# Optimization experiments

Hardware: AMD Instinct MI355X
Metric: run time of the kernel (lower is better)

The kernel has to match this reference:

```python
import jax, jax.numpy as jnp
import numpy as np

N_HEADS = 16
ROPE_THETA = 10000.0


def _rotate_half(x):
    d = x.shape[-1] // 2
    return jnp.concatenate([-x[..., d:], x[..., :d]], axis=-1)


def setup_inputs() -> dict:
    key = jax.random.key(0)
    k1, k2, k3, k4 = jax.random.split(key, 4)
    B, S, D = 2, 2048, 2048
    std = 0.02
    return {
        "x": jax.random.normal(k1, (B, S, D), dtype=jnp.float32),
        "wq": std * jax.random.normal(k2, (D, D), dtype=jnp.float32),
        "wkv": std * jax.random.normal(k3, (D, 2 * D), dtype=jnp.float32),
        "wo": std * jax.random.normal(k4, (D, D), dtype=jnp.float32),
    }


def reference(x, wq, wkv, wo):
    # prefill case: kv_cache=None, past_length=0
    B, S, D = x.shape
    H = N_HEADS
    dh = D // H

    Q = x @ wq.T                                   # [B,S,D]
    K, V = jnp.split(x @ wkv, 2, axis=-1)          # [B,S,D] each

    q = Q.reshape(B, S, H, dh).transpose(0, 2, 1, 3)  # [B,H,S,dh]
    k = K.reshape(B, S, H, dh).transpose(0, 2, 1, 3)
    v = V.reshape(B, S, H, dh).transpose(0, 2, 1, 3)

    # RoPE tables (cos/sin of outer(pos, inv_freq), duplicated across halves)
    inv_freq = 1.0 / (ROPE_THETA ** (jnp.arange(0, dh, 2, dtype=jnp.float32) / dh))
    emb = jnp.arange(S, dtype=jnp.float32)[:, None] * inv_freq[None, :]  # [S, dh/2]
    cos = jnp.tile(jnp.cos(emb), (1, 2))[None, None]  # [1,1,S,dh]
    sin = jnp.tile(jnp.sin(emb), (1, 2))[None, None]

    q = q * cos + _rotate_half(q) * sin
    k = k * cos + _rotate_half(k) * sin

    scale = 1.0 / jnp.sqrt(jnp.asarray(dh, dtype=x.dtype))
    scores = jnp.einsum('bhqd,bhkd->bhqk', q, k) * scale  # [B,H,S,S]
    causal = jnp.tril(jnp.ones((S, S), dtype=bool))
    scores = jnp.where(causal[None, None], scores, -jnp.inf)
    attn = jax.nn.softmax(scores, axis=-1)

    out = jnp.einsum('bhqk,bhkd->bhqd', attn, v)          # [B,H,S,dh]
    out = out.transpose(0, 2, 1, 3).reshape(B, S, D)
    return out @ wo.T
```

## Files before the change

kernel.cpp:

```cpp
#include <hip/hip_runtime.h>
#include <stdint.h>

typedef unsigned short u16;
typedef __attribute__((ext_vector_type(8))) short short8;
typedef __attribute__((ext_vector_type(4))) float floatx4;

#define MFMA16(a, b, c) __builtin_amdgcn_mfma_f32_16x16x32_bf16(a, b, c, 0, 0, 0)

static __device__ __forceinline__ void gl_lds16(const void* g, void* l) {
  __builtin_amdgcn_global_load_lds(
      (const __attribute__((address_space(1))) uint32_t*)g,
      (__attribute__((address_space(3))) uint32_t*)l, 16, 0, 0);
}

static __device__ __forceinline__ float b2f(u16 u) {
  union { float f; unsigned u; } v;
  v.u = ((unsigned)u) << 16;
  return v.f;
}
static __device__ __forceinline__ u16 f2b(float f) {
  union { float f; unsigned u; } v;
  v.f = f;
  unsigned r = v.u + 0x7fffu + ((v.u >> 16) & 1u);
  return (u16)(r >> 16);
}

template <int CTRL>
static __device__ __forceinline__ float dppf(float x) {
  return __builtin_bit_cast(
      float, __builtin_amdgcn_update_dpp(0, __builtin_bit_cast(int, x), CTRL,
                                         0xF, 0xF, true));
}
static __device__ __forceinline__ float sum16(float x) {
  x += dppf<0x128>(x);
  x += dppf<0x124>(x);
  x += dppf<0x122>(x);
  x += dppf<0x121>(x);
  return x;
}
static __device__ __forceinline__ float max16(float x) {
  x = fmaxf(x, dppf<0x128>(x));
  x = fmaxf(x, dppf<0x124>(x));
  x = fmaxf(x, dppf<0x122>(x));
  x = fmaxf(x, dppf<0x121>(x));
  return x;
}

__global__ __launch_bounds__(256) void detect_f32(const u16* __restrict__ x,
                                                  int* __restrict__ flag) {
  __shared__ int cnt[256];
  int c = 0;
  for (int i = threadIdx.x; i < 65536; i += 256) {
    int e = (x[i] >> 7) & 0xFF;
    if (e >= 140) ++c;
  }
  cnt[threadIdx.x] = c;
  __syncthreads();
  for (int s = 128; s > 0; s >>= 1) {
    if (threadIdx.x < (unsigned)s) cnt[threadIdx.x] += cnt[threadIdx.x + s];
    __syncthreads();
  }
  if (threadIdx.x == 0) *flag = (cnt[0] > 1000) ? 1 : 0;
}

__global__ __launch_bounds__(256) void convert_in8(const void* __restrict__ src,
                                                   u16* __restrict__ dst, int n8,
                                                   const int* __restrict__ flag) {
  int i = blockIdx.x * 256 + threadIdx.x;
  if (i >= n8) return;
  short8 r;
  if (*flag) {
    const float4* s = (const float4*)src;
    float4 a = s[2 * i], b = s[2 * i + 1];
    r[0] = (short)f2b(a.x); r[1] = (short)f2b(a.y);
    r[2] = (short)f2b(a.z); r[3] = (short)f2b(a.w);
    r[4] = (short)f2b(b.x); r[5] = (short)f2b(b.y);
    r[6] = (short)f2b(b.z); r[7] = (short)f2b(b.w);
  } else {
    r = ((const short8*)src)[i];
  }
  ((short8*)dst)[i] = r;
}

__global__ __launch_bounds__(256) void transpose_conv(const void* __restrict__ in,
                                                      u16* __restrict__ out,
                                                      int R, int Ccols,
                                                      const int* __restrict__ flag) {
  __shared__ u16 tile[32][33];
  int f = *flag;
  int c0 = blockIdx.x * 32, r0 = blockIdx.y * 32;
  int lx = threadIdx.x & 31, ly = threadIdx.x >> 5;
#pragma unroll
  for (int i = 0; i < 32; i += 8) {
    size_t idx = (size_t)(r0 + ly + i) * Ccols + c0 + lx;
    tile[ly + i][lx] = f ? f2b(((const float*)in)[idx]) : ((const u16*)in)[idx];
  }
  __syncthreads();
#pragma unroll
  for (int i = 0; i < 32; i += 8)
    out[(size_t)(c0 + ly + i) * R + r0 + lx] = tile[lx][ly + i];
}

__global__ __launch_bounds__(256) void transpose_v(const u16* __restrict__ KV,
                                                   u16* __restrict__ Vt) {
  __shared__ u16 tile[32][33];
  int b = blockIdx.z;
  int d0 = blockIdx.x * 32, s0 = blockIdx.y * 32;
  int lx = threadIdx.x & 31, ly = threadIdx.x >> 5;
  const u16* src = KV + ((size_t)(b * 2048 + s0)) * 4096 + 2048 + d0;
#pragma unroll
  for (int i = 0; i < 32; i += 8)
    tile[ly + i][lx] = src[(size_t)(ly + i) * 4096 + lx];
  __syncthreads();
  u16* dst = Vt + ((size_t)(b * 2048 + d0)) * 2048 + s0;
#pragma unroll
  for (int i = 0; i < 32; i += 8)
    dst[(size_t)(ly + i) * 2048 + lx] = tile[lx][ly + i];
}

__global__ __launch_bounds__(256) void gemm_nt(const u16* __restrict__ A,
                                               const u16* __restrict__ Bm,
                                               void* __restrict__ Cv,
                                               int M, int N, int K,
                                               const int* __restrict__ flag,
                                               int flag_mode) {
  __shared__ u16 Ash[128 * 64];
  __shared__ u16 Bsh[128 * 64];
  int tid = threadIdx.x, w = tid >> 6, lane = tid & 63;
  int quad = lane >> 4, l15 = lane & 15;
  int m0 = blockIdx.y * 128, n0 = blockIdx.x * 128;
  int wm = (w & 1) * 64, wn = (w >> 1) * 64;
  int f32out = flag_mode ? *flag : 0;

  floatx4 acc[4][4];
#pragma unroll
  for (int i = 0; i < 4; ++i)
#pragma unroll
    for (int j = 0; j < 4; ++j) acc[i][j] = floatx4{0.f, 0.f, 0.f, 0.f};

  int srow = lane >> 3;
  int gch = (lane & 7) ^ srow;
  const u16* Ag = A + (size_t)(m0 + w * 32 + srow) * K + gch * 8;
  const u16* Bg = Bm + (size_t)(n0 + w * 32 + srow) * K + gch * 8;

  for (int k0 = 0; k0 < K; k0 += 64) {
    __syncthreads();
#pragma unroll
    for (int t = 0; t < 4; ++t) {
      gl_lds16(Ag + (size_t)t * 8 * K + k0, (void*)(Ash + (w * 32 + t * 8) * 64));
      gl_lds16(Bg + (size_t)t * 8 * K + k0, (void*)(Bsh + (w * 32 + t * 8) * 64));
    }
    __syncthreads();
#pragma unroll
    for (int kk = 0; kk < 2; ++kk) {
      int c = kk * 4 + quad;
      short8 af[4], bf[4];
#pragma unroll
      for (int i = 0; i < 4; ++i) {
        int m = wm + 16 * i + l15;
        af[i] = *(const short8*)(Ash + m * 64 + ((c ^ (m & 7)) << 3));
        int n = wn + 16 * i + l15;
        bf[i] = *(const short8*)(Bsh + n * 64 + ((c ^ (n & 7)) << 3));
      }
#pragma unroll
      for (int i = 0; i < 4; ++i)
#pragma unroll
        for (int j = 0; j < 4; ++j) acc[i][j] = MFMA16(af[i], bf[j], acc[i][j]);
    }
  }

#pragma unroll
  for (int i = 0; i < 4; ++i)
#pragma unroll
    for (int r = 0; r < 4; ++r) {
      int row = m0 + wm + 16 * i + quad * 4 + r;
      if (f32out) {
        float* cp = (float*)Cv + (size_t)row * N + n0 + wn + l15;
#pragma unroll
        for (int j = 0; j < 4; ++j) cp[16 * j] = acc[i][j][r];
      } else {
        u16* cp = (u16*)Cv + (size_t)row * N + n0 + wn + l15;
#pragma unroll
        for (int j = 0; j < 4; ++j) cp[16 * j] = f2b(acc[i][j][r]);
      }
    }
}

__global__ __launch_bounds__(256) void rope_kernel(u16* __restrict__ Q,
                                                   u16* __restrict__ KV) {
  const float scale = 0.08838834764831845f;
  int idx = blockIdx.x * 256 + threadIdx.x;
  int tok = idx >> 10;
  int rem = idx & 1023;
  int h = rem >> 6, i = rem & 63;
  int pos = tok & 2047;
  float f = __powf(10000.0f, -(float)(2 * i) * (1.0f / 128.0f));
  float ang = (float)pos * f;
  float s, c;
  sincosf(ang, &s, &c);

  size_t qb = (size_t)tok * 2048 + h * 128 + i;
  float q1 = b2f(Q[qb]), q2 = b2f(Q[qb + 64]);
  Q[qb] = f2b((q1 * c - q2 * s) * scale);
  Q[qb + 64] = f2b((q2 * c + q1 * s) * scale);

  size_t kb = (size_t)tok * 4096 + h * 128 + i;
  float k1 = b2f(KV[kb]), k2 = b2f(KV[kb + 64]);
  KV[kb] = f2b(k1 * c - k2 * s);
  KV[kb + 64] = f2b(k2 * c + k1 * s);
}

__global__ __launch_bounds__(512, 1) void flash_attn(const u16* __restrict__ Q,
                                                     const u16* __restrict__ KV,
                                                     const u16* __restrict__ Vt,
                                                     u16* __restrict__ O) {
  const int S = 2048, D = 2048, KVld = 4096;
  int bh = blockIdx.x;
  int pair = blockIdx.y;
  int b = bh >> 4, h = bh & 15;
  int tid = threadIdx.x, w = tid >> 6, lane = tid & 63;
  int quad = lane >> 4, l15 = lane & 15;

  const u16* Qb = Q + (size_t)(b * S) * D + h * 128;
  const u16* Kb = KV + (size_t)(b * S) * KVld + h * 128;
  const u16* Vtb = Vt + ((size_t)(b * 2048 + h * 128)) * S;

  __shared__ u16 Ksh[64 * 128];
  __shared__ u16 Vsh[128 * 64];
  __shared__ u16 Psh[8][16 * 64];

  for (int pi = 0; pi < 2; ++pi) {
    int qt = pi ? (15 - pair) : pair;
    int q0 = qt * 128;
    int qw = q0 + w * 16;

    short8 qf[4];
    {
      const u16* qp = Qb + (size_t)(qw + l15) * D + quad * 8;
#pragma unroll
      for (int kk = 0; kk < 4; ++kk) qf[kk] = *(const short8*)(qp + kk * 32);
    }

    floatx4 o[8];
#pragma unroll
    for (int t = 0; t < 8; ++t) o[t] = floatx4{0.f, 0.f, 0.f, 0.f};
    float mrow[4], lrow[4];
#pragma unroll
    for (int r = 0; r < 4; ++r) { mrow[r] = -1e30f; lrow[r] = 0.f; }

    int nk = 2 * qt + 2;
    for (int kt = 0; kt < nk; ++kt) {
      int kb = kt * 64;
      __syncthreads();

#pragma unroll
      for (int tt = 0; tt < 2; ++tt) {
        int r0 = w * 8 + tt * 4;
        int row = r0 + quad;
        int g = (l15 & 8) | ((l15 & 7) ^ (row & 7));
        gl_lds16(Kb + (size_t)(kb + row) * KVld + g * 8, (void*)(Ksh + r0 * 128));
      }
#pragma unroll
      for (int tt = 0; tt < 2; ++tt) {
        int d0 = w * 16 + tt * 8;
        int d = d0 + (lane >> 3);
        int g = (lane & 7) ^ (d & 7);
        gl_lds16(Vtb + (size_t)d * S + kb + g * 8, (void*)(Vsh + d0 * 64));
      }
      __syncthreads();

      if (kb <= qw + 15) {
        floatx4 sc[4];
#pragma unroll
        for (int nf = 0; nf < 4; ++nf) sc[nf] = floatx4{0.f, 0.f, 0.f, 0.f};
#pragma unroll
        for (int kk = 0; kk < 4; ++kk) {
          int c = kk * 4 + quad;
          short8 kf[4];
#pragma unroll
          for (int nf = 0; nf < 4; ++nf) {
            int n = nf * 16 + l15;
            int pc = (c & 8) | ((c & 7) ^ (n & 7));
            kf[nf] = *(const short8*)(Ksh + n * 128 + pc * 8);
          }
#pragma unroll
          for (int nf = 0; nf < 4; ++nf) sc[nf] = MFMA16(qf[kk], kf[nf], sc[nf]);
        }

        bool masked = (kb + 63 > qw);
        floatx4 alv;
#pragma unroll
        for (int r = 0; r < 4; ++r) {
          int qg = qw + quad * 4 + r;
          float v0 = sc[0][r], v1 = sc[1][r];
          float v2 = sc[2][r], v3 = sc[3][r];
          if (masked) {
            v0 = (kb + l15 <= qg) ? v0 : -1e30f;
            v1 = (kb + 16 + l15 <= qg) ? v1 : -1e30f;
            v2 = (kb + 32 + l15 <= qg) ? v2 : -1e30f;
            v3 = (kb + 48 + l15 <= qg) ? v3 : -1e30f;
          }
          float mx = max16(fmaxf(fmaxf(v0, v1), fmaxf(v2, v3)));
          float mn = fmaxf(mrow[r], mx);
          float al = __expf(mrow[r] - mn);
          mrow[r] = mn;
          float p0 = __expf(v0 - mn), p1 = __expf(v1 - mn);
          float p2 = __expf(v2 - mn), p3 = __expf(v3 - mn);
          float rs = sum16((p0 + p1) + (p2 + p3));
          lrow[r] = lrow[r] * al + rs;
          alv[r] = al;
          int m_ = quad * 4 + r, sw = m_ & 7;
          int cb = l15 >> 3, e = l15 & 7;
          u16* pr = Psh[w] + m_ * 64;
          pr[(((0 + cb) ^ sw) << 3) + e] = f2b(p0);
          pr[(((2 + cb) ^ sw) << 3) + e] = f2b(p1);
          pr[(((4 + cb) ^ sw) << 3) + e] = f2b(p2);
          pr[(((6 + cb) ^ sw) << 3) + e] = f2b(p3);
        }
#pragma unroll
        for (int t = 0; t < 8; ++t) o[t] *= alv;
        __asm__ volatile("s_waitcnt lgkmcnt(0)" ::: "memory");

#pragma unroll
        for (int ks = 0; ks < 2; ++ks) {
          int c = ks * 4 + quad;
          short8 pf = *(const short8*)(Psh[w] + l15 * 64 + ((c ^ (l15 & 7)) << 3));
#pragma unroll
          for (int t = 0; t < 8; ++t) {
            int d = t * 16 + l15;
            short8 vf = *(const short8*)(Vsh + d * 64 + ((c ^ (d & 7)) << 3));
            o[t] = MFMA16(pf, vf, o[t]);
          }
        }
      }
    }

#pragma unroll
    for (int r = 0; r < 4; ++r) {
      float inv = 1.0f / lrow[r];
      int qg = qw + quad * 4 + r;
      u16* op = O + (size_t)(b * S + qg) * D + h * 128;
#pragma unroll
      for (int t = 0; t < 8; ++t) op[t * 16 + l15] = f2b(o[t][r] * inv);
    }
  }
}

extern "C" void kernel_launch(void* const* d_in, const int* in_sizes, int n_in,
                              void* d_out, int out_size, void* d_ws, size_t ws_size,
                              hipStream_t stream) {
  const void* x = d_in[0];
  const void* wq = d_in[1];
  const void* wkv = d_in[2];
  const void* wo = d_in[3];

  int* flag = (int*)d_ws;
  u16* xb = (u16*)d_ws + 64;
  u16* Wbuf = xb + (size_t)8388608;
  u16* Qb = Wbuf + (size_t)8388608;
  u16* KVb = Qb + (size_t)8388608;
  u16* AO = xb;

  detect_f32<<<1, 256, 0, stream>>>((const u16*)x, flag);
  convert_in8<<<4096, 256, 0, stream>>>(x, xb, 1048576, flag);
  convert_in8<<<2048, 256, 0, stream>>>(wq, Wbuf, 524288, flag);
  gemm_nt<<<dim3(16, 32), 256, 0, stream>>>(xb, Wbuf, Qb, 4096, 2048, 2048, flag, 0);
  transpose_conv<<<dim3(128, 64), 256, 0, stream>>>(wkv, Wbuf, 2048, 4096, flag);
  gemm_nt<<<dim3(32, 32), 256, 0, stream>>>(xb, Wbuf, KVb, 4096, 4096, 2048, flag, 0);
  transpose_v<<<dim3(64, 64, 2), 256, 0, stream>>>(KVb, Wbuf);
  rope_kernel<<<16384, 256, 0, stream>>>(Qb, KVb);
  flash_attn<<<dim3(32, 8), 512, 0, stream>>>(Qb, KVb, Wbuf, AO);
  convert_in8<<<2048, 256, 0, stream>>>(wo, Wbuf, 524288, flag);
  gemm_nt<<<dim3(16, 32), 256, 0, stream>>>(AO, Wbuf, d_out, 4096, 2048, 2048, flag, 1);
}
```

Measured before the change: 488.9 us.

## Replace GEMM with 256x256 double-buffered, 8-wave pipelined MFMA kernel

Replaces the 128x128 single-buffered GEMM with a 256x256-tile, 512-thread kernel. It double-buffers LDS, issues global-to-LDS loads in quarter stages interleaved with MFMA phases, and uses explicit waitcnt, barriers and setprio. The goal is to hide global load latency and raise arithmetic intensity per tile for the three projection GEMMs. In exchange, LDS use per block is much larger, the grid has fewer blocks (128 or 256 blocks on a large CU count), and the hand-written waitcnt and barrier scheduling is fragile.

```diff
diff --git a/kernel.cpp b/kernel.cpp
--- a/kernel.cpp
+++ b/kernel.cpp
@@ -118,59 +118,156 @@
     dst[(size_t)(ly + i) * 2048 + lx] = tile[lx][ly + i];
 }
 
-__global__ __launch_bounds__(256) void gemm_nt(const u16* __restrict__ A,
-                                               const u16* __restrict__ Bm,
-                                               void* __restrict__ Cv,
-                                               int M, int N, int K,
-                                               const int* __restrict__ flag,
-                                               int flag_mode) {
-  __shared__ u16 Ash[128 * 64];
-  __shared__ u16 Bsh[128 * 64];
+__global__ __launch_bounds__(512, 2) void gemm8(const u16* __restrict__ A,
+                                                const u16* __restrict__ Bm,
+                                                void* __restrict__ Cv,
+                                                int M, int N, int K,
+                                                const int* __restrict__ flag,
+                                                int flag_mode) {
+  __shared__ u16 Ash[2 * 256 * 64];
+  __shared__ u16 Bsh[2 * 256 * 64];
   int tid = threadIdx.x, w = tid >> 6, lane = tid & 63;
   int quad = lane >> 4, l15 = lane & 15;
-  int m0 = blockIdx.y * 128, n0 = blockIdx.x * 128;
-  int wm = (w & 1) * 64, wn = (w >> 1) * 64;
+  int wr = w >> 2, wc = w & 3;
+  int wm = wr * 128, wn = wc * 64;
+  int m0 = blockIdx.y * 256, n0 = blockIdx.x * 256;
   int f32out = flag_mode ? *flag : 0;
-
-  floatx4 acc[4][4];
-#pragma unroll
-  for (int i = 0; i < 4; ++i)
+  const int NT = K >> 6;
+
+  int srow8 = lane >> 3;
+  int gch = (lane & 7) ^ srow8;
+  const u16* Ag = A + (size_t)(m0 + w * 8 + srow8) * K + gch * 8;
+  const u16* Bg = Bm + (size_t)(n0 + w * 8 + srow8) * K + gch * 8;
+  int ldsrow = w * 8;
+
+  floatx4 acc[8][4];
+#pragma unroll
+  for (int i = 0; i < 8; ++i)
 #pragma unroll
     for (int j = 0; j < 4; ++j) acc[i][j] = floatx4{0.f, 0.f, 0.f, 0.f};
 
-  int srow = lane >> 3;
-  int gch = (lane & 7) ^ srow;
-  const u16* Ag = A + (size_t)(m0 + w * 32 + srow) * K + gch * 8;
-  const u16* Bg = Bm + (size_t)(n0 + w * 32 + srow) * K + gch * 8;
-
-  for (int k0 = 0; k0 < K; k0 += 64) {
-    __syncthreads();
-#pragma unroll
-    for (int t = 0; t < 4; ++t) {
-      gl_lds16(Ag + (size_t)t * 8 * K + k0, (void*)(Ash + (w * 32 + t * 8) * 64));
-      gl_lds16(Bg + (size_t)t * 8 * K + k0, (void*)(Bsh + (w * 32 + t * 8) * 64));
-    }
-    __syncthreads();
-#pragma unroll
-    for (int kk = 0; kk < 2; ++kk) {
-      int c = kk * 4 + quad;
-      short8 af[4], bf[4];
-#pragma unroll
-      for (int i = 0; i < 4; ++i) {
-        int m = wm + 16 * i + l15;
-        af[i] = *(const short8*)(Ash + m * 64 + ((c ^ (m & 7)) << 3));
-        int n = wn + 16 * i + l15;
-        bf[i] = *(const short8*)(Bsh + n * 64 + ((c ^ (n & 7)) << 3));
-      }
-#pragma unroll
-      for (int i = 0; i < 4; ++i)
-#pragma unroll
-        for (int j = 0; j < 4; ++j) acc[i][j] = MFMA16(af[i], bf[j], acc[i][j]);
-    }
-  }
-
-#pragma unroll
-  for (int i = 0; i < 4; ++i)
+  int ch0 = ((quad ^ (l15 & 7)) << 3);
+  int ch1 = (((4 + quad) ^ (l15 & 7)) << 3);
+
+  auto stage = [&](int qi) {
+    int tau = qi >> 2;
+    int tc = tau < NT ? tau : NT - 1;
+    int hh = qi & 3;
+    int half = (hh & 1) * 128;
+    int sbuf = (tau & 1) * (256 * 64);
+    size_t kof = (size_t)tc * 64;
+    if (hh < 2) {
+      gl_lds16(Bg + (size_t)half * K + kof,
+               (void*)(Bsh + sbuf + (half + ldsrow) * 64));
+      gl_lds16(Bg + (size_t)(half + 64) * K + kof,
+               (void*)(Bsh + sbuf + (half + 64 + ldsrow) * 64));
+    } else {
+      gl_lds16(Ag + (size_t)half * K + kof,
+               (void*)(Ash + sbuf + (half + ldsrow) * 64));
+      gl_lds16(Ag + (size_t)(half + 64) * K + kof,
+               (void*)(Ash + sbuf + (half + 64 + ldsrow) * 64));
+    }
+  };
+
+  stage(0); stage(1); stage(2); stage(3);
+  __asm__ volatile("s_waitcnt vmcnt(4)" ::: "memory");
+  stage(4); stage(5); stage(6);
+  __asm__ volatile("s_waitcnt vmcnt(6)" ::: "memory");
+  __builtin_amdgcn_s_barrier();
+
+  for (int t = 0; t < NT; ++t) {
+    u16* As = Ash + (t & 1) * (256 * 64);
+    u16* Bs = Bsh + (t & 1) * (256 * 64);
+    if (t) {
+      __asm__ volatile("s_waitcnt vmcnt(6)" ::: "memory");
+      __builtin_amdgcn_s_barrier();
+    }
+    int qb = 7 + 4 * t;
+    short8 bf[8], af0[8], af1[8];
+
+#pragma unroll
+    for (int j = 0; j < 4; ++j) {
+      int n = wn + 16 * j + l15;
+      bf[2 * j] = *(const short8*)(Bs + n * 64 + ch0);
+      bf[2 * j + 1] = *(const short8*)(Bs + n * 64 + ch1);
+    }
+#pragma unroll
+    for (int i = 0; i < 4; ++i) {
+      int m = wm + 16 * i + l15;
+      af0[2 * i] = *(const short8*)(As + m * 64 + ch0);
+      af0[2 * i + 1] = *(const short8*)(As + m * 64 + ch1);
+    }
+    stage(qb);
+    __builtin_amdgcn_s_barrier();
+    __asm__ volatile("s_waitcnt lgkmcnt(0)" ::: "memory");
+    __builtin_amdgcn_sched_barrier(0);
+    __builtin_amdgcn_s_setprio(1);
+#pragma unroll
+    for (int i = 0; i < 4; ++i)
+#pragma unroll
+      for (int j = 0; j < 2; ++j) {
+        acc[i][j] = MFMA16(af0[2 * i], bf[2 * j], acc[i][j]);
+        acc[i][j] = MFMA16(af0[2 * i + 1], bf[2 * j + 1], acc[i][j]);
+      }
+    __builtin_amdgcn_s_setprio(0);
+    __builtin_amdgcn_s_barrier();
+
+#pragma unroll
+    for (int i = 0; i < 4; ++i) {
+      int m = wm + 64 + 16 * i + l15;
+      af1[2 * i] = *(const short8*)(As + m * 64 + ch0);
+    }
+    stage(qb + 1);
+    __builtin_amdgcn_s_barrier();
+    __asm__ volatile("s_waitcnt lgkmcnt(0)" ::: "memory");
+    __builtin_amdgcn_sched_barrier(0);
+    __builtin_amdgcn_s_setprio(1);
+#pragma unroll
+    for (int i = 0; i < 4; ++i)
+#pragma unroll
+      for (int j = 2; j < 4; ++j) {
+        acc[i][j] = MFMA16(af0[2 * i], bf[2 * j], acc[i][j]);
+        acc[i][j] = MFMA16(af0[2 * i + 1], bf[2 * j + 1], acc[i][j]);
+      }
+    __builtin_amdgcn_s_setprio(0);
+    __builtin_amdgcn_s_barrier();
+
+#pragma unroll
+    for (int i = 0; i < 4; ++i) {
+      int m = wm + 64 + 16 * i + l15;
+      af1[2 * i + 1] = *(const short8*)(As + m * 64 + ch1);
+    }
+    stage(qb + 2);
+    __builtin_amdgcn_s_barrier();
+    __asm__ volatile("s_waitcnt lgkmcnt(0)" ::: "memory");
+    __builtin_amdgcn_sched_barrier(0);
+    __builtin_amdgcn_s_setprio(1);
+#pragma unroll
+    for (int i = 0; i < 4; ++i)
+#pragma unroll
+      for (int j = 0; j < 2; ++j) {
+        acc[4 + i][j] = MFMA16(af1[2 * i], bf[2 * j], acc[4 + i][j]);
+        acc[4 + i][j] = MFMA16(af1[2 * i + 1], bf[2 * j + 1], acc[4 + i][j]);
+      }
+    __builtin_amdgcn_s_setprio(0);
+    __builtin_amdgcn_s_barrier();
+
+    stage(qb + 3);
+    __builtin_amdgcn_s_barrier();
+    __builtin_amdgcn_s_setprio(1);
+#pragma unroll
+    for (int i = 0; i < 4; ++i)
+#pragma unroll
+      for (int j = 2; j < 4; ++j) {
+        acc[4 + i][j] = MFMA16(af1[2 * i], bf[2 * j], acc[4 + i][j]);
+        acc[4 + i][j] = MFMA16(af1[2 * i + 1], bf[2 * j + 1], acc[4 + i][j]);
+      }
+    __builtin_amdgcn_s_setprio(0);
+    __builtin_amdgcn_s_barrier();
+  }
+
+#pragma unroll
+  for (int i = 0; i < 8; ++i)
 #pragma unroll
     for (int r = 0; r < 4; ++r) {
       int row = m0 + wm + 16 * i + quad * 4 + r;
@@ -364,12 +461,12 @@
   detect_f32<<<1, 256, 0, stream>>>((const u16*)x, flag);
   convert_in8<<<4096, 256, 0, stream>>>(x, xb, 1048576, flag);
   convert_in8<<<2048, 256, 0, stream>>>(wq, Wbuf, 524288, flag);
-  gemm_nt<<<dim3(16, 32), 256, 0, stream>>>(xb, Wbuf, Qb, 4096, 2048, 2048, flag, 0);
+  gemm8<<<dim3(8, 16), 512, 0, stream>>>(xb, Wbuf, Qb, 4096, 2048, 2048, flag, 0);
   transpose_conv<<<dim3(128, 64), 256, 0, stream>>>(wkv, Wbuf, 2048, 4096, flag);
-  gemm_nt<<<dim3(32, 32), 256, 0, stream>>>(xb, Wbuf, KVb, 4096, 4096, 2048, flag, 0);
+  gemm8<<<dim3(16, 16), 512, 0, stream>>>(xb, Wbuf, KVb, 4096, 4096, 2048, flag, 0);
   transpose_v<<<dim3(64, 64, 2), 256, 0, stream>>>(KVb, Wbuf);
   rope_kernel<<<16384, 256, 0, stream>>>(Qb, KVb);
   flash_attn<<<dim3(32, 8), 512, 0, stream>>>(Qb, KVb, Wbuf, AO);
   convert_in8<<<2048, 256, 0, stream>>>(wo, Wbuf, 524288, flag);
-  gemm_nt<<<dim3(16, 32), 256, 0, stream>>>(AO, Wbuf, d_out, 4096, 2048, 2048, flag, 1);
-}
+  gemm8<<<dim3(8, 16), 512, 0, stream>>>(AO, Wbuf, d_out, 4096, 2048, 2048, flag, 1);
+}
```

Result: slower. 525.3 us (+7.4%).
